# Kernel optimization log

Hardware: AMD Instinct MI355X
Metric: run time of the kernel (lower is better)

Reference implementation:

```python
import jax, jax.numpy as jnp
import numpy as np

TOP_K = 5
TRUNC = 100
EPS = 1e-07
B, T_STEPS, I_DIM, H_DIM, N_CLS = 32, 384, 64, 128, 10


def setup_inputs() -> dict:
    key = jax.random.key(0)
    ks = jax.random.split(key, 8)
    s = 1.0 / np.sqrt(H_DIM)
    u = lambda k, sh: jax.random.uniform(k, sh, jnp.float32, -s, s)
    return {
        "x": jax.random.normal(ks[0], (B, T_STEPS, I_DIM), jnp.float32),
        "W_ih": u(ks[1], (4 * H_DIM, I_DIM)),
        "W_hh": u(ks[2], (4 * H_DIM, H_DIM)),
        "b_ih": u(ks[3], (4 * H_DIM,)),
        "b_hh": u(ks[4], (4 * H_DIM,)),
        "w_t": jax.random.normal(ks[5], (2 * H_DIM, 1), jnp.float32) * 0.01,
        "W_fc": u(ks[6], (N_CLS, 2 * H_DIM)),
        "b_fc": u(ks[7], (N_CLS,)),
    }


def _lstm_cell(x_t, h, c, W_ih, W_hh, b_ih, b_hh):
    # torch.nn.LSTMCell: gate order i, f, g, o
    g = x_t @ W_ih.T + b_ih + h @ W_hh.T + b_hh
    i, f, gg, o = jnp.split(g, 4, axis=1)
    c = jax.nn.sigmoid(f) * c + jax.nn.sigmoid(i) * jnp.tanh(gg)
    h = jax.nn.sigmoid(o) * jnp.tanh(c)
    return h, c


def _sparse_attn(scores, mask, r):
    # scores: [B, T+1]; mask: valid-prefix bool [T+1]; r: traced valid length
    Bsz, L = scores.shape
    neg = jnp.where(mask[None, :], scores, -jnp.inf)

    def small(_):
        return jax.nn.softmax(neg, axis=1)

    def big(_):
        delta = jax.lax.top_k(neg, TOP_K)[0][:, -1] + EPS  # [B], k-th largest
        # faithful to torch: delta.repeat((1, r)).view(B, r) -> delta[(b*r+t) % B]
        dmat = delta[(jnp.arange(Bsz)[:, None] * r + jnp.arange(L)[None, :]) % Bsz]
        w = jnp.clip(scores - dmat, 0.0, None) * mask[None, :]
        return w / (jnp.sum(w, axis=1, keepdims=True) + EPS)

    return jax.lax.cond(r <= TOP_K, small, big, None)


def reference(x, W_ih, W_hh, b_ih, b_hh, w_t, W_fc, b_fc):
    Bsz, T, _ = x.shape
    H = W_hh.shape[1]
    dt = x.dtype
    buf0 = jnp.zeros((Bsz, T + 1, H), dt)  # h_old buffer; slot 0 (zeros) is valid
    pos = jnp.arange(T + 1)

    def step(carry, inp):
        h, c, buf = carry
        i, x_t = inp
        h, c = jax.lax.cond(
            (i + 1) % TRUNC == 0,
            lambda hc: (jax.lax.stop_gradient(hc[0]), jax.lax.stop_gradient(hc[1])),
            lambda hc: hc,
            (h, c),
        )
        h, c = _lstm_cell(x_t, h, c, W_ih, W_hh, b_ih, b_hh)
        r = i + 1  # remember_size (valid prefix of buf)
        mask = (pos < r).astype(dt)  # [T+1]
        mlp = jnp.tanh(jnp.concatenate(
            (jnp.broadcast_to(h[:, None, :], buf.shape), buf), axis=2))  # [B,T+1,2H]
        scores = (mlp @ w_t)[..., 0]  # [B, T+1]
        attn = _sparse_attn(scores, mask, r)  # [B, T+1], zero on invalid slots
        attn_c = jnp.einsum('bt,bth->bh', attn, buf)
        h = h + attn_c
        buf = jax.lax.dynamic_update_slice(buf, h[:, None, :], (0, r, 0))
        return (h, c, buf), (h, attn_c)

    init = (jnp.zeros((Bsz, H), dt), jnp.zeros((Bsz, H), dt), buf0)
    _, (hs, attn_all) = jax.lax.scan(step, init, (jnp.arange(T), jnp.swapaxes(x, 0, 1)))
    outputs = jnp.concatenate(
        (jnp.swapaxes(hs, 0, 1), jnp.swapaxes(attn_all, 0, 1)), axis=2)  # [B,T,2H]
    out = outputs @ W_fc.T + b_fc  # [B, T, num_classes]
    return out, jnp.swapaxes(hs, 0, 1)
```

## Files before the change

kernel.cpp:

```cpp
#include <hip/hip_runtime.h>
#include <stdint.h>

typedef unsigned long long u64;

#define NB   32
#define TST  384
#define IDM  64
#define HDM  128
#define NCLS 10
#define EPSF 1e-7f
#define LOG2E 1.44269504088896340736f

#define O_SBUF 0
#define O_WLDS 388
#define O_ACT  776
#define O_GEX  968
#define O_RED4 1480
#define O_DELT 2504
#define O_WFC  2536
#define O_BFC  5176
#define O_MISC 5188
#define SMTOT  5220

__device__ __forceinline__ float sigm(float x) {
  return 1.0f / (1.0f + __builtin_amdgcn_exp2f(-LOG2E * x));
}
__device__ __forceinline__ float tanh_f(float x) {
  return 1.0f - 2.0f / (1.0f + __builtin_amdgcn_exp2f(2.0f * LOG2E * x));
}

__global__ __launch_bounds__(512, 2)
void sab_kernel(const float* __restrict__ x, const float* __restrict__ Wih,
                const float* __restrict__ Whh, const float* __restrict__ bihp,
                const float* __restrict__ bhhp, const float* __restrict__ wtp,
                const float* __restrict__ Wfcp, const float* __restrict__ bfcp,
                float* __restrict__ dout, u64* __restrict__ mail) {
  __shared__ __align__(16) float SM[SMTOT];
  int* IMISC = (int*)(SM + O_MISC);
  int* IDX   = (int*)(SM + O_GEX);

  const int tid  = threadIdx.x;
  const int lane = tid & 63;
  const int wvid = tid >> 6;
  const int b    = blockIdx.x;
  const int go   = tid >> 3;
  const int kc   = tid & 7;

  float* hsout = dout + (size_t)NB * TST * NCLS;
  const float* myx = x + (size_t)b * TST * IDM;

  float w[8][24];
  #pragma unroll
  for (int i = 0; i < 8; ++i) {
    const int g = 8 * go + i;
    #pragma unroll
    for (int j = 0; j < 24; ++j) {
      const int k = 24 * kc + j;
      const float* sp = (k < IDM) ? (Wih + g * IDM + k) : (Whh + g * HDM + (k - IDM));
      w[i][j] = *sp;
    }
  }
  const float bias = bihp[tid] + bhhp[tid];
  float wt0 = 0.f, wt1 = 0.f, cst = 0.f;
  if (tid < HDM) { wt0 = wtp[tid]; wt1 = wtp[HDM + tid]; }

  float t5a = 0.f, t5b = -3e38f, t5c = -3e38f, t5d = -3e38f, t5e = -3e38f;

  for (int idx = tid; idx < NCLS * 256; idx += 512) {
    const int c = idx >> 8, k = idx & 255;
    SM[O_WFC + c * 264 + k] = Wfcp[idx];
  }
  if (tid < NCLS) SM[O_BFC + tid] = bfcp[tid];
  if (tid < HDM) SM[O_ACT + 64 + tid] = 0.f;
  if (tid < IDM) SM[O_ACT + tid] = myx[tid];
  if (tid == 0) {
    SM[O_SBUF] = 0.f;
    __hip_atomic_store(&mail[b],      0ull, __ATOMIC_RELAXED, __HIP_MEMORY_SCOPE_AGENT);
    __hip_atomic_store(&mail[NB + b], 0ull, __ATOMIC_RELAXED, __HIP_MEMORY_SCOPE_AGENT);
  }
  __syncthreads();

  float hc = 0.f;
  for (int t = 0; t < TST; ++t) {
    const int r = t + 1;

    float acc[8] = {0,0,0,0,0,0,0,0};
    {
      const float4* a4 = reinterpret_cast<const float4*>(SM + O_ACT + kc * 24);
      #pragma unroll
      for (int m = 0; m < 6; ++m) {
        const float4 av = a4[m];
        #pragma unroll
        for (int i = 0; i < 8; ++i) {
          acc[i] = fmaf(av.x, w[i][4*m+0], acc[i]);
          acc[i] = fmaf(av.y, w[i][4*m+1], acc[i]);
          acc[i] = fmaf(av.z, w[i][4*m+2], acc[i]);
          acc[i] = fmaf(av.w, w[i][4*m+3], acc[i]);
        }
      }
    }
    #pragma unroll
    for (int i = 0; i < 8; ++i) {
      acc[i] += __shfl_xor(acc[i], 1, 64);
      acc[i] += __shfl_xor(acc[i], 2, 64);
      acc[i] += __shfl_xor(acc[i], 4, 64);
    }
    float pre = acc[0];
    #pragma unroll
    for (int i = 1; i < 8; ++i) if (kc == i) pre = acc[i];
    pre += bias;
    const bool tg = (tid >= 256) && (tid < 384);
    SM[O_GEX + tid] = tg ? tanh_f(pre) : sigm(pre);
    __syncthreads();

    float th = 0.f;
    if (tid < HDM) {
      const float iv = SM[O_GEX + tid];
      const float fv = SM[O_GEX + 128 + tid];
      const float gv = SM[O_GEX + 256 + tid];
      const float ov = SM[O_GEX + 384 + tid];
      cst = fv * cst + iv * gv;
      hc  = ov * tanh_f(cst);
      th  = tanh_f(hc) * wt0;
    }
    #pragma unroll
    for (int s = 1; s < 64; s <<= 1) th += __shfl_xor(th, s, 64);
    if (lane == 0 && tid < HDM) SM[O_MISC + wvid] = th;
    __syncthreads();
    const float s_h = SM[O_MISC] + SM[O_MISC + 1];

    const bool big = (r > 5);
    if (big) {
      if (tid == 0) {
        const float delta = t5e + s_h + EPSF;
        const u64 pv = (((u64)(unsigned)r) << 32) | (u64)__float_as_uint(delta);
        __hip_atomic_store(&mail[(r & 1) * NB + b], pv, __ATOMIC_RELEASE, __HIP_MEMORY_SCOPE_AGENT);
      }
      if (tid < NB) {
        u64* slot = &mail[(r & 1) * NB + tid];
        u64 v = __hip_atomic_load(slot, __ATOMIC_ACQUIRE, __HIP_MEMORY_SCOPE_AGENT);
        while ((unsigned)(v >> 32) != (unsigned)r) {
          __builtin_amdgcn_s_sleep(2);
          v = __hip_atomic_load(slot, __ATOMIC_ACQUIRE, __HIP_MEMORY_SCOPE_AGENT);
        }
        SM[O_DELT + tid] = __uint_as_float((unsigned)v);
      }
    }
    __syncthreads();

    float wval = 0.f;
    bool pred = false;
    if (big) {
      if (tid < r) {
        const int base = (b * r) & (NB - 1);
        const float sc = s_h + SM[O_SBUF + tid];
        wval = fmaxf(sc - SM[O_DELT + ((base + tid) & (NB - 1))], 0.f);
        SM[O_WLDS + tid] = wval;
        pred = (wval > 0.f) && (tid > 0);
      }
    } else {
      float scv = (tid < r) ? (s_h + SM[O_SBUF + tid]) : -3e38f;
      float mx = scv;
      #pragma unroll
      for (int s = 1; s < 64; s <<= 1) mx = fmaxf(mx, __shfl_xor(mx, s, 64));
      if (tid < r) {
        wval = __builtin_amdgcn_exp2f(LOG2E * (scv - mx));
        SM[O_WLDS + tid] = wval;
        pred = (tid > 0);
      }
    }
    float wsp = wval;
    #pragma unroll
    for (int s = 1; s < 64; s <<= 1) wsp += __shfl_xor(wsp, s, 64);
    if (lane == 0) SM[O_MISC + 2 + wvid] = wsp;
    const u64 bmask = __ballot((int)pred);
    if (lane == 0) IMISC[16 + wvid] = (int)__popcll(bmask);
    __syncthreads();

    float wsum = 0.f;
    #pragma unroll
    for (int i = 0; i < 8; ++i) wsum += SM[O_MISC + 2 + i];
    const float inv = 1.0f / (wsum + (big ? EPSF : 0.f));
    int wbase = 0, nnz = 0;
    #pragma unroll
    for (int i = 0; i < 8; ++i) {
      const int c = IMISC[16 + i];
      if (i < wvid) wbase += c;
      nnz += c;
    }
    if (pred) {
      const int pos = wbase + (int)__popcll(bmask & ((1ull << lane) - 1ull));
      IDX[pos] = tid;
    }
    __syncthreads();

    const int j8 = tid & 15, q = tid >> 4;
    float ac[8] = {0,0,0,0,0,0,0,0};
    for (int ii = q; ii < nnz; ii += 32) {
      const int tp = IDX[ii];
      const float wgt = SM[O_WLDS + tp] * inv;
      const float* bp = hsout + ((size_t)(b * TST + tp - 1)) * HDM + j8 * 8;
      const float4 v0 = *reinterpret_cast<const float4*>(bp);
      const float4 v1 = *reinterpret_cast<const float4*>(bp + 4);
      ac[0] = fmaf(wgt, v0.x, ac[0]); ac[1] = fmaf(wgt, v0.y, ac[1]);
      ac[2] = fmaf(wgt, v0.z, ac[2]); ac[3] = fmaf(wgt, v0.w, ac[3]);
      ac[4] = fmaf(wgt, v1.x, ac[4]); ac[5] = fmaf(wgt, v1.y, ac[5]);
      ac[6] = fmaf(wgt, v1.z, ac[6]); ac[7] = fmaf(wgt, v1.w, ac[7]);
    }
    #pragma unroll
    for (int i = 0; i < 8; ++i) {
      ac[i] += __shfl_xor(ac[i], 16, 64);
      ac[i] += __shfl_xor(ac[i], 32, 64);
    }
    if ((q & 3) == 0) {
      float4* r4 = reinterpret_cast<float4*>(SM + O_RED4 + wvid * 128 + j8 * 8);
      r4[0] = make_float4(ac[0], ac[1], ac[2], ac[3]);
      r4[1] = make_float4(ac[4], ac[5], ac[6], ac[7]);
    }
    __syncthreads();

    float tb = 0.f;
    if (tid < HDM) {
      float s = 0.f;
      #pragma unroll
      for (int wv2 = 0; wv2 < 8; ++wv2) s += SM[O_RED4 + wv2 * 128 + tid];
      const float hf = hc + s;
      hsout[((size_t)(b * TST + t)) * HDM + tid] = hf;
      SM[O_ACT + 64 + tid] = hf;
      SM[O_GEX + tid] = hf;
      SM[O_GEX + 128 + tid] = s;
      tb = tanh_f(hf) * wt1;
    }
    if (tid < IDM && t + 1 < TST) SM[O_ACT + tid] = myx[(size_t)(t + 1) * IDM + tid];
    #pragma unroll
    for (int s2 = 1; s2 < 64; s2 <<= 1) tb += __shfl_xor(tb, s2, 64);
    if (lane == 0 && tid < HDM) SM[O_MISC + 24 + wvid] = tb;
    __syncthreads();

    if (tid == 0 && r < TST) {
      const float sb = SM[O_MISC + 24] + SM[O_MISC + 25];
      SM[O_SBUF + r] = sb;
      if (sb > t5e) {
        if (sb > t5a)      { t5e=t5d; t5d=t5c; t5c=t5b; t5b=t5a; t5a=sb; }
        else if (sb > t5b) { t5e=t5d; t5d=t5c; t5c=t5b; t5b=sb; }
        else if (sb > t5c) { t5e=t5d; t5d=t5c; t5c=sb; }
        else if (sb > t5d) { t5e=t5d; t5d=sb; }
        else               { t5e=sb; }
      }
    }
    if (tid < 160) {
      const int cls = tid >> 4, p = tid & 15;
      float pt = 0.f;
      #pragma unroll
      for (int i = 0; i < 16; ++i) {
        const int k = p + 16 * i;
        pt = fmaf(SM[O_WFC + cls * 264 + k], SM[O_GEX + k], pt);
      }
      #pragma unroll
      for (int s2 = 1; s2 < 16; s2 <<= 1) pt += __shfl_xor(pt, s2, 64);
      if (p == 0) dout[((size_t)(b * TST + t)) * NCLS + cls] = pt + SM[O_BFC + cls];
    }
    __syncthreads();
  }
}

extern "C" void kernel_launch(void* const* d_in, const int* in_sizes, int n_in,
                              void* d_out, int out_size, void* d_ws, size_t ws_size,
                              hipStream_t stream) {
  const float* x   = (const float*)d_in[0];
  const float* Wih = (const float*)d_in[1];
  const float* Whh = (const float*)d_in[2];
  const float* bih = (const float*)d_in[3];
  const float* bhh = (const float*)d_in[4];
  const float* wt  = (const float*)d_in[5];
  const float* Wfc = (const float*)d_in[6];
  const float* bfc = (const float*)d_in[7];
  sab_kernel<<<dim3(NB), dim3(512), 0, stream>>>(
      x, Wih, Whh, bih, bhh, wt, Wfc, bfc, (float*)d_out, (u64*)d_ws);
}
```

Before: 2.116 ms.

## Restructure LSTM step to cut barriers: per-thread gates, ballot gather, deferred FC

Reassigns gate rows so each 4-thread group owns all four gates of one hidden unit, computing the cell update in registers without an LDS gate exchange and barrier. The sparse attention gather now walks the ballot mask per wave with shuffles instead of building a compacted index list, which removes the prefix-count barrier. The score-buffer/top-5 update and the FC output are deferred into the start of the next step, and the final FC is emitted after the loop. Mailbox slots are padded to separate cache lines and use relaxed atomics with a shorter sleep. This cuts the per-step barrier count, at the cost of weaker memory ordering on the cross-block exchange and a possibly less balanced gather.

```diff
diff --git a/kernel.cpp b/kernel.cpp
--- a/kernel.cpp
+++ b/kernel.cpp
@@ -12,15 +12,14 @@
 #define LOG2E 1.44269504088896340736f
 
 #define O_SBUF 0
-#define O_WLDS 388
-#define O_ACT  776
-#define O_GEX  968
-#define O_RED4 1480
-#define O_DELT 2504
-#define O_WFC  2536
-#define O_BFC  5176
-#define O_MISC 5188
-#define SMTOT  5220
+#define O_DELT 388
+#define O_MISC 420
+#define O_ACT  452
+#define O_GEX  644
+#define O_RED  900
+#define O_WFC  1924
+#define O_BFC  4564
+#define SMTOT  4576
 
 __device__ __forceinline__ float sigm(float x) {
   return 1.0f / (1.0f + __builtin_amdgcn_exp2f(-LOG2E * x));
@@ -28,239 +27,212 @@
 __device__ __forceinline__ float tanh_f(float x) {
   return 1.0f - 2.0f / (1.0f + __builtin_amdgcn_exp2f(2.0f * LOG2E * x));
 }
-
-__global__ __launch_bounds__(512, 2)
+__device__ __forceinline__ float wave_sum(float v) {
+  v += __shfl_xor(v, 1, 64);  v += __shfl_xor(v, 2, 64);
+  v += __shfl_xor(v, 4, 64);  v += __shfl_xor(v, 8, 64);
+  v += __shfl_xor(v, 16, 64); v += __shfl_xor(v, 32, 64);
+  return v;
+}
+
+__global__ __attribute__((amdgpu_waves_per_eu(2, 2))) __launch_bounds__(512)
 void sab_kernel(const float* __restrict__ x, const float* __restrict__ Wih,
                 const float* __restrict__ Whh, const float* __restrict__ bihp,
                 const float* __restrict__ bhhp, const float* __restrict__ wtp,
                 const float* __restrict__ Wfcp, const float* __restrict__ bfcp,
                 float* __restrict__ dout, u64* __restrict__ mail) {
   __shared__ __align__(16) float SM[SMTOT];
-  int* IMISC = (int*)(SM + O_MISC);
-  int* IDX   = (int*)(SM + O_GEX);
 
   const int tid  = threadIdx.x;
   const int lane = tid & 63;
-  const int wvid = tid >> 6;
+  const int wv   = tid >> 6;
   const int b    = blockIdx.x;
-  const int go   = tid >> 3;
-  const int kc   = tid & 7;
+  const int j    = tid >> 2;
+  const int s    = tid & 3;
 
   float* hsout = dout + (size_t)NB * TST * NCLS;
   const float* myx = x + (size_t)b * TST * IDM;
 
-  float w[8][24];
+  float w[4][48];
+  float bias[4];
   #pragma unroll
-  for (int i = 0; i < 8; ++i) {
-    const int g = 8 * go + i;
-    #pragma unroll
-    for (int j = 0; j < 24; ++j) {
-      const int k = 24 * kc + j;
-      const float* sp = (k < IDM) ? (Wih + g * IDM + k) : (Whh + g * HDM + (k - IDM));
-      w[i][j] = *sp;
-    }
-  }
-  const float bias = bihp[tid] + bhhp[tid];
-  float wt0 = 0.f, wt1 = 0.f, cst = 0.f;
-  if (tid < HDM) { wt0 = wtp[tid]; wt1 = wtp[HDM + tid]; }
+  for (int g = 0; g < 4; ++g) {
+    const int row = g * HDM + j;
+    #pragma unroll
+    for (int kk = 0; kk < 48; ++kk) {
+      const int k = 48 * s + kk;
+      w[g][kk] = (k < IDM) ? Wih[row * IDM + k] : Whh[row * HDM + (k - IDM)];
+    }
+    bias[g] = bihp[row] + bhhp[row];
+  }
+  const float wt0 = wtp[j];
+  const float wt1 = wtp[HDM + j];
 
   float t5a = 0.f, t5b = -3e38f, t5c = -3e38f, t5d = -3e38f, t5e = -3e38f;
 
-  for (int idx = tid; idx < NCLS * 256; idx += 512) {
-    const int c = idx >> 8, k = idx & 255;
-    SM[O_WFC + c * 264 + k] = Wfcp[idx];
-  }
+  for (int i = tid; i < SMTOT; i += 512) SM[i] = 0.f;
+  __syncthreads();
+  for (int idx = tid; idx < NCLS * 256; idx += 512)
+    SM[O_WFC + (idx >> 8) * 264 + (idx & 255)] = Wfcp[idx];
   if (tid < NCLS) SM[O_BFC + tid] = bfcp[tid];
-  if (tid < HDM) SM[O_ACT + 64 + tid] = 0.f;
-  if (tid < IDM) SM[O_ACT + tid] = myx[tid];
+  if (tid < IDM)  SM[O_ACT + tid] = myx[tid];
   if (tid == 0) {
-    SM[O_SBUF] = 0.f;
-    __hip_atomic_store(&mail[b],      0ull, __ATOMIC_RELAXED, __HIP_MEMORY_SCOPE_AGENT);
-    __hip_atomic_store(&mail[NB + b], 0ull, __ATOMIC_RELAXED, __HIP_MEMORY_SCOPE_AGENT);
+    __hip_atomic_store(&mail[(0 * NB + b) * 8], 0ull, __ATOMIC_RELAXED, __HIP_MEMORY_SCOPE_AGENT);
+    __hip_atomic_store(&mail[(1 * NB + b) * 8], 0ull, __ATOMIC_RELAXED, __HIP_MEMORY_SCOPE_AGENT);
   }
   __syncthreads();
 
-  float hc = 0.f;
+  float cst = 0.f, hc = 0.f;
+
   for (int t = 0; t < TST; ++t) {
     const int r = t + 1;
-
-    float acc[8] = {0,0,0,0,0,0,0,0};
+    const bool big = (r > 5);
+
+    if (t > 0) {
+      if (tid == 0) {
+        float sb = 0.f;
+        #pragma unroll
+        for (int i = 0; i < 8; ++i) sb += SM[O_MISC + 16 + i];
+        SM[O_SBUF + t] = sb;
+        if (sb > t5e) {
+          if (sb > t5a)      { t5e=t5d; t5d=t5c; t5c=t5b; t5b=t5a; t5a=sb; }
+          else if (sb > t5b) { t5e=t5d; t5d=t5c; t5c=t5b; t5b=sb; }
+          else if (sb > t5c) { t5e=t5d; t5d=t5c; t5c=sb; }
+          else if (sb > t5d) { t5e=t5d; t5d=sb; }
+          else               { t5e=sb; }
+        }
+      }
+      if (tid < 160) {
+        const int cls = tid >> 4, p = tid & 15;
+        float pt = 0.f;
+        #pragma unroll
+        for (int i = 0; i < 16; ++i) {
+          const int k = p + 16 * i;
+          pt = fmaf(SM[O_WFC + cls * 264 + k], SM[O_GEX + k], pt);
+        }
+        pt += __shfl_xor(pt, 1, 64); pt += __shfl_xor(pt, 2, 64);
+        pt += __shfl_xor(pt, 4, 64); pt += __shfl_xor(pt, 8, 64);
+        if (p == 0) dout[(size_t)(b * TST + (t - 1)) * NCLS + cls] = pt + SM[O_BFC + cls];
+      }
+    }
+
+    float a0 = 0.f, a1 = 0.f, a2 = 0.f, a3 = 0.f;
     {
-      const float4* a4 = reinterpret_cast<const float4*>(SM + O_ACT + kc * 24);
+      const float4* a4 = reinterpret_cast<const float4*>(SM + O_ACT + 48 * s);
       #pragma unroll
-      for (int m = 0; m < 6; ++m) {
+      for (int m = 0; m < 12; ++m) {
         const float4 av = a4[m];
-        #pragma unroll
-        for (int i = 0; i < 8; ++i) {
-          acc[i] = fmaf(av.x, w[i][4*m+0], acc[i]);
-          acc[i] = fmaf(av.y, w[i][4*m+1], acc[i]);
-          acc[i] = fmaf(av.z, w[i][4*m+2], acc[i]);
-          acc[i] = fmaf(av.w, w[i][4*m+3], acc[i]);
-        }
-      }
-    }
-    #pragma unroll
-    for (int i = 0; i < 8; ++i) {
-      acc[i] += __shfl_xor(acc[i], 1, 64);
-      acc[i] += __shfl_xor(acc[i], 2, 64);
-      acc[i] += __shfl_xor(acc[i], 4, 64);
-    }
-    float pre = acc[0];
-    #pragma unroll
-    for (int i = 1; i < 8; ++i) if (kc == i) pre = acc[i];
-    pre += bias;
-    const bool tg = (tid >= 256) && (tid < 384);
-    SM[O_GEX + tid] = tg ? tanh_f(pre) : sigm(pre);
-    __syncthreads();
-
-    float th = 0.f;
-    if (tid < HDM) {
-      const float iv = SM[O_GEX + tid];
-      const float fv = SM[O_GEX + 128 + tid];
-      const float gv = SM[O_GEX + 256 + tid];
-      const float ov = SM[O_GEX + 384 + tid];
-      cst = fv * cst + iv * gv;
-      hc  = ov * tanh_f(cst);
-      th  = tanh_f(hc) * wt0;
-    }
-    #pragma unroll
-    for (int s = 1; s < 64; s <<= 1) th += __shfl_xor(th, s, 64);
-    if (lane == 0 && tid < HDM) SM[O_MISC + wvid] = th;
-    __syncthreads();
-    const float s_h = SM[O_MISC] + SM[O_MISC + 1];
-
-    const bool big = (r > 5);
+        a0 = fmaf(av.x, w[0][4*m+0], a0); a0 = fmaf(av.y, w[0][4*m+1], a0);
+        a0 = fmaf(av.z, w[0][4*m+2], a0); a0 = fmaf(av.w, w[0][4*m+3], a0);
+        a1 = fmaf(av.x, w[1][4*m+0], a1); a1 = fmaf(av.y, w[1][4*m+1], a1);
+        a1 = fmaf(av.z, w[1][4*m+2], a1); a1 = fmaf(av.w, w[1][4*m+3], a1);
+        a2 = fmaf(av.x, w[2][4*m+0], a2); a2 = fmaf(av.y, w[2][4*m+1], a2);
+        a2 = fmaf(av.z, w[2][4*m+2], a2); a2 = fmaf(av.w, w[2][4*m+3], a2);
+        a3 = fmaf(av.x, w[3][4*m+0], a3); a3 = fmaf(av.y, w[3][4*m+1], a3);
+        a3 = fmaf(av.z, w[3][4*m+2], a3); a3 = fmaf(av.w, w[3][4*m+3], a3);
+      }
+    }
+    a0 += __shfl_xor(a0, 1, 64); a0 += __shfl_xor(a0, 2, 64);
+    a1 += __shfl_xor(a1, 1, 64); a1 += __shfl_xor(a1, 2, 64);
+    a2 += __shfl_xor(a2, 1, 64); a2 += __shfl_xor(a2, 2, 64);
+    a3 += __shfl_xor(a3, 1, 64); a3 += __shfl_xor(a3, 2, 64);
+    const float iv = sigm(a0 + bias[0]);
+    const float fv = sigm(a1 + bias[1]);
+    const float gv = tanh_f(a2 + bias[2]);
+    const float ov = sigm(a3 + bias[3]);
+    cst = fv * cst + iv * gv;
+    hc  = ov * tanh_f(cst);
+
+    const float shp = wave_sum((s == 0) ? tanh_f(hc) * wt0 : 0.f);
+    if (lane == 0) SM[O_MISC + wv] = shp;
+    __syncthreads();
+
+    float s_h = 0.f;
+    #pragma unroll
+    for (int i = 0; i < 8; ++i) s_h += SM[O_MISC + i];
+
     if (big) {
       if (tid == 0) {
-        const float delta = t5e + s_h + EPSF;
-        const u64 pv = (((u64)(unsigned)r) << 32) | (u64)__float_as_uint(delta);
-        __hip_atomic_store(&mail[(r & 1) * NB + b], pv, __ATOMIC_RELEASE, __HIP_MEMORY_SCOPE_AGENT);
+        const u64 pv = (((u64)(unsigned)r) << 32) | (u64)__float_as_uint(t5e + s_h + EPSF);
+        __hip_atomic_store(&mail[((r & 1) * NB + b) * 8], pv, __ATOMIC_RELAXED, __HIP_MEMORY_SCOPE_AGENT);
       }
       if (tid < NB) {
-        u64* slot = &mail[(r & 1) * NB + tid];
-        u64 v = __hip_atomic_load(slot, __ATOMIC_ACQUIRE, __HIP_MEMORY_SCOPE_AGENT);
+        u64* slot = &mail[((r & 1) * NB + tid) * 8];
+        u64 v = __hip_atomic_load(slot, __ATOMIC_RELAXED, __HIP_MEMORY_SCOPE_AGENT);
         while ((unsigned)(v >> 32) != (unsigned)r) {
-          __builtin_amdgcn_s_sleep(2);
-          v = __hip_atomic_load(slot, __ATOMIC_ACQUIRE, __HIP_MEMORY_SCOPE_AGENT);
+          __builtin_amdgcn_s_sleep(1);
+          v = __hip_atomic_load(slot, __ATOMIC_RELAXED, __HIP_MEMORY_SCOPE_AGENT);
         }
         SM[O_DELT + tid] = __uint_as_float((unsigned)v);
       }
     }
-    __syncthreads();
-
-    float wval = 0.f;
-    bool pred = false;
+    const float sc = s_h + SM[O_SBUF + tid];
+    __syncthreads();
+
+    float wval = 0.f; bool pred = false;
     if (big) {
       if (tid < r) {
-        const int base = (b * r) & (NB - 1);
-        const float sc = s_h + SM[O_SBUF + tid];
-        wval = fmaxf(sc - SM[O_DELT + ((base + tid) & (NB - 1))], 0.f);
-        SM[O_WLDS + tid] = wval;
+        wval = fmaxf(sc - SM[O_DELT + ((b * r + tid) & (NB - 1))], 0.f);
         pred = (wval > 0.f) && (tid > 0);
       }
     } else {
-      float scv = (tid < r) ? (s_h + SM[O_SBUF + tid]) : -3e38f;
+      float scv = (tid < r) ? sc : -3e38f;
       float mx = scv;
-      #pragma unroll
-      for (int s = 1; s < 64; s <<= 1) mx = fmaxf(mx, __shfl_xor(mx, s, 64));
+      mx = fmaxf(mx, __shfl_xor(mx, 1, 64));  mx = fmaxf(mx, __shfl_xor(mx, 2, 64));
+      mx = fmaxf(mx, __shfl_xor(mx, 4, 64));  mx = fmaxf(mx, __shfl_xor(mx, 8, 64));
+      mx = fmaxf(mx, __shfl_xor(mx, 16, 64)); mx = fmaxf(mx, __shfl_xor(mx, 32, 64));
       if (tid < r) {
         wval = __builtin_amdgcn_exp2f(LOG2E * (scv - mx));
-        SM[O_WLDS + tid] = wval;
         pred = (tid > 0);
       }
     }
-    float wsp = wval;
-    #pragma unroll
-    for (int s = 1; s < 64; s <<= 1) wsp += __shfl_xor(wsp, s, 64);
-    if (lane == 0) SM[O_MISC + 2 + wvid] = wsp;
-    const u64 bmask = __ballot((int)pred);
-    if (lane == 0) IMISC[16 + wvid] = (int)__popcll(bmask);
+    const u64 m0 = __ballot((int)pred);
+    const float wsp = wave_sum(wval);
+    if (lane == 0) SM[O_MISC + 8 + wv] = wsp;
+
+    float g0 = 0.f, g1 = 0.f;
+    u64 m = m0;
+    while (m) {
+      const int l = __builtin_ctzll(m); m &= m - 1;
+      const float wgt = __shfl(wval, l, 64);
+      const int tp = (wv << 6) + l;
+      const float2 v = reinterpret_cast<const float2*>(hsout + (size_t)(b * TST + tp - 1) * HDM)[lane];
+      g0 = fmaf(wgt, v.x, g0); g1 = fmaf(wgt, v.y, g1);
+    }
+    reinterpret_cast<float2*>(SM + O_RED + wv * HDM)[lane] = make_float2(g0, g1);
     __syncthreads();
 
     float wsum = 0.f;
     #pragma unroll
-    for (int i = 0; i < 8; ++i) wsum += SM[O_MISC + 2 + i];
-    const float inv = 1.0f / (wsum + (big ? EPSF : 0.f));
-    int wbase = 0, nnz = 0;
-    #pragma unroll
-    for (int i = 0; i < 8; ++i) {
-      const int c = IMISC[16 + i];
-      if (i < wvid) wbase += c;
-      nnz += c;
-    }
-    if (pred) {
-      const int pos = wbase + (int)__popcll(bmask & ((1ull << lane) - 1ull));
-      IDX[pos] = tid;
-    }
-    __syncthreads();
-
-    const int j8 = tid & 15, q = tid >> 4;
-    float ac[8] = {0,0,0,0,0,0,0,0};
-    for (int ii = q; ii < nnz; ii += 32) {
-      const int tp = IDX[ii];
-      const float wgt = SM[O_WLDS + tp] * inv;
-      const float* bp = hsout + ((size_t)(b * TST + tp - 1)) * HDM + j8 * 8;
-      const float4 v0 = *reinterpret_cast<const float4*>(bp);
-      const float4 v1 = *reinterpret_cast<const float4*>(bp + 4);
-      ac[0] = fmaf(wgt, v0.x, ac[0]); ac[1] = fmaf(wgt, v0.y, ac[1]);
-      ac[2] = fmaf(wgt, v0.z, ac[2]); ac[3] = fmaf(wgt, v0.w, ac[3]);
-      ac[4] = fmaf(wgt, v1.x, ac[4]); ac[5] = fmaf(wgt, v1.y, ac[5]);
-      ac[6] = fmaf(wgt, v1.z, ac[6]); ac[7] = fmaf(wgt, v1.w, ac[7]);
-    }
-    #pragma unroll
-    for (int i = 0; i < 8; ++i) {
-      ac[i] += __shfl_xor(ac[i], 16, 64);
-      ac[i] += __shfl_xor(ac[i], 32, 64);
-    }
-    if ((q & 3) == 0) {
-      float4* r4 = reinterpret_cast<float4*>(SM + O_RED4 + wvid * 128 + j8 * 8);
-      r4[0] = make_float4(ac[0], ac[1], ac[2], ac[3]);
-      r4[1] = make_float4(ac[4], ac[5], ac[6], ac[7]);
-    }
-    __syncthreads();
-
-    float tb = 0.f;
-    if (tid < HDM) {
-      float s = 0.f;
-      #pragma unroll
-      for (int wv2 = 0; wv2 < 8; ++wv2) s += SM[O_RED4 + wv2 * 128 + tid];
-      const float hf = hc + s;
-      hsout[((size_t)(b * TST + t)) * HDM + tid] = hf;
-      SM[O_ACT + 64 + tid] = hf;
-      SM[O_GEX + tid] = hf;
-      SM[O_GEX + 128 + tid] = s;
-      tb = tanh_f(hf) * wt1;
+    for (int i = 0; i < 8; ++i) wsum += SM[O_MISC + 8 + i];
+    const float inv = 1.0f / (wsum + (big ? EPSF : 0.0f));
+    float attn = 0.f;
+    #pragma unroll
+    for (int wv2 = 0; wv2 < 8; ++wv2) attn += SM[O_RED + wv2 * HDM + j];
+    attn *= inv;
+    const float hf = hc + attn;
+    if (s == 0) {
+      SM[O_ACT + IDM + j] = hf;
+      SM[O_GEX + j] = hf;
+      SM[O_GEX + HDM + j] = attn;
+      hsout[(size_t)(b * TST + t) * HDM + j] = hf;
     }
     if (tid < IDM && t + 1 < TST) SM[O_ACT + tid] = myx[(size_t)(t + 1) * IDM + tid];
-    #pragma unroll
-    for (int s2 = 1; s2 < 64; s2 <<= 1) tb += __shfl_xor(tb, s2, 64);
-    if (lane == 0 && tid < HDM) SM[O_MISC + 24 + wvid] = tb;
-    __syncthreads();
-
-    if (tid == 0 && r < TST) {
-      const float sb = SM[O_MISC + 24] + SM[O_MISC + 25];
-      SM[O_SBUF + r] = sb;
-      if (sb > t5e) {
-        if (sb > t5a)      { t5e=t5d; t5d=t5c; t5c=t5b; t5b=t5a; t5a=sb; }
-        else if (sb > t5b) { t5e=t5d; t5d=t5c; t5c=t5b; t5b=sb; }
-        else if (sb > t5c) { t5e=t5d; t5d=t5c; t5c=sb; }
-        else if (sb > t5d) { t5e=t5d; t5d=sb; }
-        else               { t5e=sb; }
-      }
-    }
-    if (tid < 160) {
-      const int cls = tid >> 4, p = tid & 15;
-      float pt = 0.f;
-      #pragma unroll
-      for (int i = 0; i < 16; ++i) {
-        const int k = p + 16 * i;
-        pt = fmaf(SM[O_WFC + cls * 264 + k], SM[O_GEX + k], pt);
-      }
-      #pragma unroll
-      for (int s2 = 1; s2 < 16; s2 <<= 1) pt += __shfl_xor(pt, s2, 64);
-      if (p == 0) dout[((size_t)(b * TST + t)) * NCLS + cls] = pt + SM[O_BFC + cls];
-    }
-    __syncthreads();
+    const float tbv = wave_sum((s == 0) ? tanh_f(hf) * wt1 : 0.f);
+    if (lane == 0) SM[O_MISC + 16 + wv] = tbv;
+    __syncthreads();
+  }
+
+  if (tid < 160) {
+    const int cls = tid >> 4, p = tid & 15;
+    float pt = 0.f;
+    #pragma unroll
+    for (int i = 0; i < 16; ++i) {
+      const int k = p + 16 * i;
+      pt = fmaf(SM[O_WFC + cls * 264 + k], SM[O_GEX + k], pt);
+    }
+    pt += __shfl_xor(pt, 1, 64); pt += __shfl_xor(pt, 2, 64);
+    pt += __shfl_xor(pt, 4, 64); pt += __shfl_xor(pt, 8, 64);
+    if (p == 0) dout[(size_t)(b * TST + (TST - 1)) * NCLS + cls] = pt + SM[O_BFC + cls];
   }
 }
 
```

Measured after the change: 3.619 ms. +71.1%, slower.

## Overlap FC output and x prefetch with cross-block mailbox spin wait

Applied to the files above, without the earlier changes.

Moves the per-step FC output projection into the window between publishing delta and spinning on the mailbox, so each step computes the previous step's logits while waiting on other blocks. This removes one __syncthreads per step, and the last step's output is emitted after the loop. The gate buffer moves to the reduction region so the FC input in O_GEX survives until the next step. The next x row is prefetched into a register during the wait, and the mailbox atomics are replaced by inline-asm sc0 sc1 global loads and stores polled by a single wave. The risk is memory-ordering correctness, since the explicit release/acquire semantics are replaced by cache-bypassing asm.

```diff
diff --git a/kernel.cpp b/kernel.cpp
--- a/kernel.cpp
+++ b/kernel.cpp
@@ -15,7 +15,7 @@
 #define O_WLDS 388
 #define O_ACT  776
 #define O_GEX  968
-#define O_RED4 1480
+#define O_RED  1480
 #define O_DELT 2504
 #define O_WFC  2536
 #define O_BFC  5176
@@ -27,6 +27,18 @@
 }
 __device__ __forceinline__ float tanh_f(float x) {
   return 1.0f - 2.0f / (1.0f + __builtin_amdgcn_exp2f(2.0f * LOG2E * x));
+}
+
+__device__ __forceinline__ void mail_store(u64* p, u64 v) {
+  asm volatile("global_store_dwordx2 %0, %1, off sc0 sc1"
+               :: "v"(p), "v"(v) : "memory");
+}
+__device__ __forceinline__ u64 mail_load(u64* p) {
+  u64 v;
+  asm volatile("global_load_dwordx2 %0, %1, off sc0 sc1\n\t"
+               "s_waitcnt vmcnt(0)"
+               : "=v"(v) : "v"(p) : "memory");
+  return v;
 }
 
 __global__ __launch_bounds__(512, 2)
@@ -75,14 +87,15 @@
   if (tid < IDM) SM[O_ACT + tid] = myx[tid];
   if (tid == 0) {
     SM[O_SBUF] = 0.f;
-    __hip_atomic_store(&mail[b],      0ull, __ATOMIC_RELAXED, __HIP_MEMORY_SCOPE_AGENT);
-    __hip_atomic_store(&mail[NB + b], 0ull, __ATOMIC_RELAXED, __HIP_MEMORY_SCOPE_AGENT);
+    mail_store(&mail[b], 0ull);
+    mail_store(&mail[NB + b], 0ull);
   }
   __syncthreads();
 
   float hc = 0.f;
   for (int t = 0; t < TST; ++t) {
     const int r = t + 1;
+    const bool big = (r > 5);
 
     float acc[8] = {0,0,0,0,0,0,0,0};
     {
@@ -110,15 +123,15 @@
     for (int i = 1; i < 8; ++i) if (kc == i) pre = acc[i];
     pre += bias;
     const bool tg = (tid >= 256) && (tid < 384);
-    SM[O_GEX + tid] = tg ? tanh_f(pre) : sigm(pre);
+    SM[O_RED + tid] = tg ? tanh_f(pre) : sigm(pre);
     __syncthreads();
 
     float th = 0.f;
     if (tid < HDM) {
-      const float iv = SM[O_GEX + tid];
-      const float fv = SM[O_GEX + 128 + tid];
-      const float gv = SM[O_GEX + 256 + tid];
-      const float ov = SM[O_GEX + 384 + tid];
+      const float iv = SM[O_RED + tid];
+      const float fv = SM[O_RED + 128 + tid];
+      const float gv = SM[O_RED + 256 + tid];
+      const float ov = SM[O_RED + 384 + tid];
       cst = fv * cst + iv * gv;
       hc  = ov * tanh_f(cst);
       th  = tanh_f(hc) * wt0;
@@ -129,22 +142,35 @@
     __syncthreads();
     const float s_h = SM[O_MISC] + SM[O_MISC + 1];
 
-    const bool big = (r > 5);
-    if (big) {
-      if (tid == 0) {
-        const float delta = t5e + s_h + EPSF;
-        const u64 pv = (((u64)(unsigned)r) << 32) | (u64)__float_as_uint(delta);
-        __hip_atomic_store(&mail[(r & 1) * NB + b], pv, __ATOMIC_RELEASE, __HIP_MEMORY_SCOPE_AGENT);
-      }
-      if (tid < NB) {
-        u64* slot = &mail[(r & 1) * NB + tid];
-        u64 v = __hip_atomic_load(slot, __ATOMIC_ACQUIRE, __HIP_MEMORY_SCOPE_AGENT);
-        while ((unsigned)(v >> 32) != (unsigned)r) {
-          __builtin_amdgcn_s_sleep(2);
-          v = __hip_atomic_load(slot, __ATOMIC_ACQUIRE, __HIP_MEMORY_SCOPE_AGENT);
-        }
-        SM[O_DELT + tid] = __uint_as_float((unsigned)v);
-      }
+    if (big && tid == 0) {
+      const float delta = t5e + s_h + EPSF;
+      const u64 pv = (((u64)(unsigned)r) << 32) | (u64)__float_as_uint(delta);
+      mail_store(&mail[(r & 1) * NB + b], pv);
+    }
+
+    float xr = 0.f;
+    if (tid < IDM && t + 1 < TST) xr = myx[(size_t)(t + 1) * IDM + tid];
+    if (t > 0 && tid < 160) {
+      const int cls = tid >> 4, p = tid & 15;
+      float pt = 0.f;
+      #pragma unroll
+      for (int i = 0; i < 16; ++i) {
+        const int k = p + 16 * i;
+        pt = fmaf(SM[O_WFC + cls * 264 + k], SM[O_GEX + k], pt);
+      }
+      #pragma unroll
+      for (int s2 = 1; s2 < 16; s2 <<= 1) pt += __shfl_xor(pt, s2, 64);
+      if (p == 0) dout[((size_t)(b * TST + (t - 1))) * NCLS + cls] = pt + SM[O_BFC + cls];
+    }
+
+    if (big && wvid == 7 && lane < NB) {
+      u64* slot = &mail[(r & 1) * NB + lane];
+      u64 v = mail_load(slot);
+      while ((unsigned)(v >> 32) != (unsigned)r) {
+        __builtin_amdgcn_s_sleep(2);
+        v = mail_load(slot);
+      }
+      SM[O_DELT + lane] = __uint_as_float((unsigned)v);
     }
     __syncthreads();
 
@@ -152,9 +178,8 @@
     bool pred = false;
     if (big) {
       if (tid < r) {
-        const int base = (b * r) & (NB - 1);
         const float sc = s_h + SM[O_SBUF + tid];
-        wval = fmaxf(sc - SM[O_DELT + ((base + tid) & (NB - 1))], 0.f);
+        wval = fmaxf(sc - SM[O_DELT + ((b * r + tid) & (NB - 1))], 0.f);
         SM[O_WLDS + tid] = wval;
         pred = (wval > 0.f) && (tid > 0);
       }
@@ -213,7 +238,7 @@
       ac[i] += __shfl_xor(ac[i], 32, 64);
     }
     if ((q & 3) == 0) {
-      float4* r4 = reinterpret_cast<float4*>(SM + O_RED4 + wvid * 128 + j8 * 8);
+      float4* r4 = reinterpret_cast<float4*>(SM + O_RED + wvid * 128 + j8 * 8);
       r4[0] = make_float4(ac[0], ac[1], ac[2], ac[3]);
       r4[1] = make_float4(ac[4], ac[5], ac[6], ac[7]);
     }
@@ -223,7 +248,7 @@
     if (tid < HDM) {
       float s = 0.f;
       #pragma unroll
-      for (int wv2 = 0; wv2 < 8; ++wv2) s += SM[O_RED4 + wv2 * 128 + tid];
+      for (int wv2 = 0; wv2 < 8; ++wv2) s += SM[O_RED + wv2 * 128 + tid];
       const float hf = hc + s;
       hsout[((size_t)(b * TST + t)) * HDM + tid] = hf;
       SM[O_ACT + 64 + tid] = hf;
@@ -231,7 +256,7 @@
       SM[O_GEX + 128 + tid] = s;
       tb = tanh_f(hf) * wt1;
     }
-    if (tid < IDM && t + 1 < TST) SM[O_ACT + tid] = myx[(size_t)(t + 1) * IDM + tid];
+    if (tid < IDM && t + 1 < TST) SM[O_ACT + tid] = xr;
     #pragma unroll
     for (int s2 = 1; s2 < 64; s2 <<= 1) tb += __shfl_xor(tb, s2, 64);
     if (lane == 0 && tid < HDM) SM[O_MISC + 24 + wvid] = tb;
@@ -248,19 +273,19 @@
         else               { t5e=sb; }
       }
     }
-    if (tid < 160) {
-      const int cls = tid >> 4, p = tid & 15;
-      float pt = 0.f;
-      #pragma unroll
-      for (int i = 0; i < 16; ++i) {
-        const int k = p + 16 * i;
-        pt = fmaf(SM[O_WFC + cls * 264 + k], SM[O_GEX + k], pt);
-      }
-      #pragma unroll
-      for (int s2 = 1; s2 < 16; s2 <<= 1) pt += __shfl_xor(pt, s2, 64);
-      if (p == 0) dout[((size_t)(b * TST + t)) * NCLS + cls] = pt + SM[O_BFC + cls];
-    }
-    __syncthreads();
+  }
+
+  if (tid < 160) {
+    const int cls = tid >> 4, p = tid & 15;
+    float pt = 0.f;
+    #pragma unroll
+    for (int i = 0; i < 16; ++i) {
+      const int k = p + 16 * i;
+      pt = fmaf(SM[O_WFC + cls * 264 + k], SM[O_GEX + k], pt);
+    }
+    #pragma unroll
+    for (int s2 = 1; s2 < 16; s2 <<= 1) pt += __shfl_xor(pt, s2, 64);
+    if (p == 0) dout[((size_t)(b * TST + (TST - 1))) * NCLS + cls] = pt + SM[O_BFC + cls];
   }
 }
 
```

New measurement: 1.893 ms, median of 2. -10.5%, faster.
